# Kernel tuning notes

Hardware: AMD Instinct MI355X
Metric: run time of the kernel (lower is better)

The kernel has to match this reference:

```python
import jax, jax.numpy as jnp
import numpy as np

BITS = 4
GROUP = 128
PACK = 32 // BITS  # 8 values per int32
MASK = (1 << BITS) - 1


def _unpack_weight(qweight, K, N):
    # qweight: [K//PACK, N] int32; PACK 4-bit values packed along K in each int32
    shifts = jnp.arange(PACK, dtype=jnp.int32) * BITS  # [PACK]
    w = (qweight[:, None, :] >> shifts[None, :, None]) & MASK  # [K//PACK, PACK, N]
    return w.reshape(K, N)


def _unpack_zeros(qzeros, G, N):
    # qzeros: [G, N//PACK] int32; PACK 4-bit values packed along N in each int32
    shifts = jnp.arange(PACK, dtype=jnp.int32) * BITS  # [PACK]
    z = (qzeros[:, :, None] >> shifts[None, None, :]) & MASK  # [G, N//PACK, PACK]
    return z.reshape(G, N)


def setup_inputs() -> dict:
    key = jax.random.key(0)
    k1, k2, k3, k4 = jax.random.split(key, 4)
    B, S, K, N = 4, 1024, 4096, 11008
    G = K // GROUP
    x = jax.random.normal(k1, (B, S, K), dtype=jnp.float32)
    qweight = jax.random.randint(k2, (K // PACK, N), 0, 2147483647, dtype=jnp.int32)
    qzeros = jax.random.randint(k3, (G, N // PACK), 0, 2147483647, dtype=jnp.int32)
    scales = jax.random.uniform(k4, (G, N), dtype=jnp.float32) * 0.01
    return {"x": x, "qweight": qweight, "qzeros": qzeros, "scales": scales}


def reference(x, qweight, qzeros, scales):
    K = x.shape[-1]
    G, N = scales.shape
    # dequantize: W[k, n] = (q[k, n] - zero[g(k), n]) * scale[g(k), n]
    w_q = _unpack_weight(qweight, K, N).astype(jnp.float32)   # [K, N]
    zeros = _unpack_zeros(qzeros, G, N).astype(jnp.float32)   # [G, N]
    gid = jnp.arange(K) // GROUP                              # [K]
    W = (w_q - zeros[gid]) * scales[gid]                      # [K, N]
    return jnp.einsum('bsk,kn->bsn', x, W)
```

## Files before the change

### kernel.cpp

```cpp
#include <hip/hip_runtime.h>


#define BK 32
#define LDK 40
#define TILE_BYTES 10240

typedef _Float16 v8h __attribute__((ext_vector_type(8)));
typedef _Float16 half2v __attribute__((ext_vector_type(2)));
typedef float v4f __attribute__((ext_vector_type(4)));

__device__ __forceinline__ unsigned pkrtz_u32(float a, float b) {
  return __builtin_bit_cast(unsigned, __builtin_amdgcn_cvt_pkrtz(a, b));
}

__device__ __forceinline__ void load_lds_16B(const void* g, void* l) {
  __builtin_amdgcn_global_load_lds(
      (const __attribute__((address_space(1))) unsigned*)g,
      (__attribute__((address_space(3))) unsigned*)l, 16, 0, 0);
}

__device__ __forceinline__ void bar() { asm volatile("s_barrier" ::: "memory"); }

__global__ __launch_bounds__(512)
void prep_ab(const float* __restrict__ x,
             const unsigned* __restrict__ qweight,
             const unsigned* __restrict__ qzeros,
             const float* __restrict__ scales,
             unsigned short* __restrict__ fa,
             unsigned short* __restrict__ fb, int M, int N, int K) {
  const int KT = K / 64;
  const int NA = (M / 256) * KT;
  int b = blockIdx.x;
  if (b < NA) {
    const int mt = b / KT, t = b - mt * KT;
    unsigned short* tile = fa + (size_t)(mt * KT + t) * 16384;
#pragma unroll
    for (int p = 0; p < 4; ++p) {
      const int c = threadIdx.x + p * 512;
      const int h = c >> 10, r = (c >> 3) & 127, s = c & 7;
      const float* src = x + (size_t)(mt * 256 + h * 128 + r) * K + t * 64 + s * 8;
      const float4 v0 = ((const float4*)src)[0];
      const float4 v1 = ((const float4*)src)[1];
      uint4 o;
      o.x = pkrtz_u32(v0.x, v0.y); o.y = pkrtz_u32(v0.z, v0.w);
      o.z = pkrtz_u32(v1.x, v1.y); o.w = pkrtz_u32(v1.z, v1.w);
      *(uint4*)(tile + h * 8192 + r * 64 + ((s ^ (r & 7)) << 3)) = o;
    }
  } else {
    b -= NA;
    const int nt = b / KT, t = b - nt * KT;
    const int g = t >> 1;
    unsigned short* tile = fb + (size_t)(nt * KT + t) * 16384;
#pragma unroll
    for (int p = 0; p < 4; ++p) {
      const int c = threadIdx.x + p * 512;
      const int h = c >> 10, r = (c >> 3) & 127, s = c & 7;
      const int n = nt * 256 + h * 128 + r;
      const unsigned zp = qzeros[(size_t)g * (N >> 3) + (n >> 3)];
      const float sc = scales[(size_t)g * N + n];
      const unsigned z = (zp >> ((n & 7) * 4)) & 15u;
      const unsigned hz_u = 0x64006400u | z | (z << 16);
      const half2v hz2 = __builtin_bit_cast(half2v, hz_u);
      const half2v hs2 = __builtin_bit_cast(half2v, pkrtz_u32(sc, sc));
      const unsigned qv = qweight[(size_t)(t * 8 + s) * N + n];
      uint4 o;
      unsigned* wp = (unsigned*)&o;
#pragma unroll
      for (int bb = 0; bb < 4; ++bb) {
        const unsigned byte = qv >> (8 * bb);
        const unsigned pq = 0x64006400u | (byte & 0xFu) | ((byte & 0xF0u) << 12);
        const half2v w2 = (__builtin_bit_cast(half2v, pq) - hz2) * hs2;
        wp[bb] = __builtin_bit_cast(unsigned, w2);
      }
      *(uint4*)(tile + h * 8192 + r * 64 + ((s ^ (r & 7)) << 3)) = o;
    }
  }
}


#define READA4(PA, MB)                                                         \
  _Pragma("unroll") for (int i = 0; i < 4; ++i) {                              \
    aF[i][0] = *(const v8h*)((PA) + ((MB + i) * 16 + lr16) * 128 + koff0);     \
    aF[i][1] = *(const v8h*)((PA) + ((MB + i) * 16 + lr16) * 128 + koff1);     \
  }

#define READB2(PB, BF, NB)                                                     \
  _Pragma("unroll") for (int j = 0; j < 2; ++j) {                              \
    BF[j][0] = *(const v8h*)((PB) + ((NB + j) * 16 + lr16) * 128 + koff0);     \
    BF[j][1] = *(const v8h*)((PB) + ((NB + j) * 16 + lr16) * 128 + koff1);     \
  }

#define MMAQ(MB, NB, BF)                                                       \
  __builtin_amdgcn_s_setprio(1);                                              \
  _Pragma("unroll") for (int i = 0; i < 4; ++i)                                \
  _Pragma("unroll") for (int j = 0; j < 2; ++j) {                              \
    acc[MB + i][NB + j] = __builtin_amdgcn_mfma_f32_16x16x32_f16(              \
        aF[i][0], BF[j][0], acc[MB + i][NB + j], 0, 0, 0);                     \
    acc[MB + i][NB + j] = __builtin_amdgcn_mfma_f32_16x16x32_f16(              \
        aF[i][1], BF[j][1], acc[MB + i][NB + j], 0, 0, 0);                     \
  }                                                                            \
  __builtin_amdgcn_s_setprio(0);

__global__ __launch_bounds__(512, 2)
void qgemm8(const unsigned short* __restrict__ fa,
            const unsigned short* __restrict__ fb,
            float* __restrict__ out, int M, int N, int K) {
  __shared__ __align__(16) short As[2][2][128][64];
  __shared__ __align__(16) short Bs[2][2][128][64];

  const int tid = threadIdx.x;
  const int lane = tid & 63;
  const int wid = tid >> 6;
  const int wr = wid >> 2, wc = wid & 3;
  const int lr16 = lane & 15, hi4 = lane >> 4, l7 = lane & 7;
  const int koff0 = ((hi4 ^ l7) << 4);
  const int koff1 = (((4 + hi4) ^ l7) << 4);

  const int nmt = M / 256;
  const int nwg = nmt * (N / 256);
  int bid = blockIdx.x;
  {
    const int xcd = bid & 7, idx = bid >> 3;
    const int q = nwg >> 3, r = nwg & 7;
    bid = (xcd < r ? xcd * (q + 1) : r * (q + 1) + (xcd - r) * q) + idx;
  }
  const int mt = bid % nmt;
  const int nt = bid / nmt;

  const int NT = K / 64;
  const int NI = NT / 2;

  const char* srcA = (const char*)fa + (size_t)mt * NT * 32768 + wid * 1024 + lane * 16;
  const char* srcB = (const char*)fb + (size_t)nt * NT * 32768 + wid * 1024 + lane * 16;
  char* ldsA = (char*)&As[0][0][0][0];
  char* ldsB = (char*)&Bs[0][0][0][0];
  char* dstA = ldsA + wid * 1024;
  char* dstB = ldsB + wid * 1024;

  auto stageA = [&](int T, int h) {
    const char* s = srcA + (size_t)T * 32768 + h * 16384;
    char* d = dstA + (T & 1) * 32768 + h * 16384;
    load_lds_16B(s, d);
    load_lds_16B(s + 8192, d + 8192);
  };
  auto stageB = [&](int T, int h) {
    const char* s = srcB + (size_t)T * 32768 + h * 16384;
    char* d = dstB + (T & 1) * 32768 + h * 16384;
    load_lds_16B(s, d);
    load_lds_16B(s + 8192, d + 8192);
  };

  const char* pA[2] = {ldsA + wr * 16384, ldsA + 32768 + wr * 16384};
  const char* pB[2] = {ldsB + (wc >> 1) * 16384 + (wc & 1) * 8192,
                       ldsB + 32768 + (wc >> 1) * 16384 + (wc & 1) * 8192};

  v4f acc[8][4] = {};
  v8h aF[4][2], bL[2][2], bH[2][2];

  stageB(0, 0); stageB(0, 1); stageA(0, 0); stageA(0, 1);
  stageB(1, 0); stageB(1, 1);
  asm volatile("s_waitcnt vmcnt(4)");
  bar();

  for (int it = 0; it < NI; ++it) {
    const int t0 = 2 * it, t1 = 2 * it + 1;
    const bool pf = (it < NI - 1);

    READA4(pA[0], 0);
    READB2(pB[0], bL, 0);
    stageA(t1, 0);
    bar();
    MMAQ(0, 0, bL);
    READB2(pB[0], bH, 2);
    stageA(t1, 1);
    bar();
    MMAQ(0, 2, bH);
    READA4(pA[0], 4);
    bar();
    MMAQ(4, 0, bL);
    if (pf) { stageB(t0 + 2, 0); stageB(t0 + 2, 1);
              asm volatile("s_waitcnt vmcnt(4)"); }
    else    { asm volatile("s_waitcnt vmcnt(0)"); }
    bar();
    MMAQ(4, 2, bH);

    READA4(pA[1], 0);
    READB2(pB[1], bL, 0);
    if (pf) stageA(t0 + 2, 0);
    bar();
    MMAQ(0, 0, bL);
    READB2(pB[1], bH, 2);
    if (pf) stageA(t0 + 2, 1);
    bar();
    MMAQ(0, 2, bH);
    READA4(pA[1], 4);
    bar();
    MMAQ(4, 0, bL);
    if (pf) { stageB(t1 + 2, 0); stageB(t1 + 2, 1);
              asm volatile("s_waitcnt vmcnt(4)"); }
    else    { asm volatile("s_waitcnt vmcnt(0)"); }
    bar();
    MMAQ(4, 2, bH);
  }

  const int m0 = mt * 256 + wr * 128;
  const int n0 = nt * 256 + wc * 64;
#pragma unroll
  for (int mi = 0; mi < 8; ++mi) {
#pragma unroll
    for (int ni = 0; ni < 4; ++ni) {
#pragma unroll
      for (int r = 0; r < 4; ++r) {
        const int row = m0 + mi * 16 + hi4 * 4 + r;
        const int col = n0 + ni * 16 + lr16;
        out[(size_t)row * N + col] = acc[mi][ni][r];
      }
    }
  }
}

__global__ __launch_bounds__(320)
void prep_x(const float* __restrict__ x, unsigned short* __restrict__ xt, int K) {
  const int kt = blockIdx.x, mt = blockIdx.y;
  unsigned short* tile = xt + (size_t)(mt * (K / 32) + kt) * (TILE_BYTES / 2);
#pragma unroll
  for (int p = 0; p < 2; ++p) {
    const int c = threadIdx.x + p * 320;
    const int r = c / 5, j = c - r * 5;
    uint4 o = {0u, 0u, 0u, 0u};
    if (j < 4) {
      const float* src = x + (size_t)(mt * 128 + r) * K + kt * 32 + j * 8;
      const float4 v0 = ((const float4*)src)[0];
      const float4 v1 = ((const float4*)src)[1];
      o.x = pkrtz_u32(v0.x, v0.y); o.y = pkrtz_u32(v0.z, v0.w);
      o.z = pkrtz_u32(v1.x, v1.y); o.w = pkrtz_u32(v1.z, v1.w);
    }
    *(uint4*)((char*)tile + (size_t)c * 16) = o;
  }
}

__global__ __launch_bounds__(512, 4)
void qgemm_dma(const unsigned short* __restrict__ xt,
               const unsigned* __restrict__ qweight,
               const unsigned* __restrict__ qzeros,
               const float* __restrict__ scales,
               float* __restrict__ out, int M, int N, int K) {
  __shared__ __align__(16) short As[128][LDK];
  __shared__ __align__(16) short Bs[256][LDK];

  const int tid = threadIdx.x;
  const int lane = tid & 63;
  const int wid = tid >> 6;
  const int n0 = blockIdx.x * 256;
  const int m0 = blockIdx.y * 128;
  const int mt = blockIdx.y;
  const int wm = (wid >> 2) * 64;
  const int wn = (wid & 3) * 64;
  const int lr = lane & 15;
  const int lk = (lane >> 4) * 8;

  const int b_n = tid & 255;
  const int b_kr0 = tid >> 8;
  const int gn = n0 + b_n;
  const unsigned* qwb = qweight + (size_t)b_kr0 * N + gn;

  const char* xt_b = (const char*)xt;
  const int NT = K / BK;

  v4f acc[4][4] = {};

  unsigned b0c, b1c, zpc;
  float scc;
  auto load_b = [&](int t, unsigned& b0, unsigned& b1, unsigned& zp, float& sc) {
    const int kk = t * BK;
    const size_t qoff = (size_t)(kk >> 3) * N;
    b0 = qwb[qoff];
    b1 = qwb[qoff + 2 * (size_t)N];
    const int g = kk >> 7;
    zp = qzeros[(size_t)g * (N >> 3) + (gn >> 3)];
    sc = scales[(size_t)g * N + gn];
  };
  load_b(0, b0c, b1c, zpc, scc);

#pragma unroll 2
  for (int t = 0; t < NT; ++t) {
    {
      const char* g = xt_b + (size_t)(mt * NT + t) * TILE_BYTES +
                      (size_t)wid * 1024 + (size_t)lane * 16;
      char* l = ((char*)&As[0][0]) + wid * 1024;
      load_lds_16B(g, l);
      if (wid < 2) load_lds_16B(g + 8 * 1024, l + 8 * 1024);
    }
    {
      const unsigned z = (zpc >> ((gn & 7) * 4)) & 15u;
      const unsigned hz_u = 0x64006400u | z | (z << 16);
      const half2v hz2 = __builtin_bit_cast(half2v, hz_u);
      const half2v hs2 = __builtin_bit_cast(half2v, pkrtz_u32(scc, scc));
      const unsigned qvs[2] = {b0c, b1c};
#pragma unroll
      for (int q = 0; q < 2; ++q) {
        const int kr = b_kr0 + q * 2;
        const unsigned qv = qvs[q];
        uint4 wv;
        unsigned* wp = (unsigned*)&wv;
#pragma unroll
        for (int j = 0; j < 4; ++j) {
          const unsigned byte = qv >> (8 * j);
          const unsigned pq = 0x64006400u | (byte & 0xFu) | ((byte & 0xF0u) << 12);
          const half2v w2 = (__builtin_bit_cast(half2v, pq) - hz2) * hs2;
          wp[j] = __builtin_bit_cast(unsigned, w2);
        }
        *(uint4*)(&Bs[b_n][kr * 8]) = wv;
      }
    }

    __syncthreads();

    unsigned b0n, b1n, zpn;
    float scn;
    const int tn = (t + 1 < NT) ? (t + 1) : t;
    load_b(tn, b0n, b1n, zpn, scn);

    v8h af[4], bfr[4];
#pragma unroll
    for (int i = 0; i < 4; ++i) {
      af[i] = *(const v8h*)(&As[wm + i * 16 + lr][lk]);
      bfr[i] = *(const v8h*)(&Bs[wn + i * 16 + lr][lk]);
    }
#pragma unroll
    for (int mi = 0; mi < 4; ++mi) {
#pragma unroll
      for (int ni = 0; ni < 4; ++ni) {
        acc[mi][ni] = __builtin_amdgcn_mfma_f32_16x16x32_f16(
            af[mi], bfr[ni], acc[mi][ni], 0, 0, 0);
      }
    }

    __syncthreads();

    b0c = b0n; b1c = b1n; zpc = zpn; scc = scn;
  }

#pragma unroll
  for (int mi = 0; mi < 4; ++mi) {
#pragma unroll
    for (int ni = 0; ni < 4; ++ni) {
#pragma unroll
      for (int r = 0; r < 4; ++r) {
        const int row = m0 + wm + mi * 16 + (lane >> 4) * 4 + r;
        const int col = n0 + wn + ni * 16 + lr;
        out[(size_t)row * N + col] = acc[mi][ni][r];
      }
    }
  }
}

__global__ __launch_bounds__(256, 2)
void qgemm_fused(const float* __restrict__ x,
                 const unsigned* __restrict__ qweight,
                 const unsigned* __restrict__ qzeros,
                 const float* __restrict__ scales,
                 float* __restrict__ out, int M, int N, int K) {
  __shared__ short As[128][LDK];
  __shared__ short Bs[128][LDK];

  const int tid = threadIdx.x;
  const int lane = tid & 63;
  const int wid = tid >> 6;
  const int n0 = blockIdx.x * 128;
  const int m0 = blockIdx.y * 128;
  const int wm = (wid >> 1) * 64;
  const int wn = (wid & 1) * 64;
  const int lr = lane & 15;
  const int lk = (lane >> 4) * 8;

  const int a_row = tid >> 3;
  const int a_col = (tid & 7) * 4;
  const int b_n = tid & 127;
  const int b_kr0 = tid >> 7;
  const int gn = n0 + b_n;

  const float* xb = x + (size_t)(m0 + a_row) * K + a_col;
  const unsigned* qwb = qweight + (size_t)b_kr0 * N + gn;

  v4f acc[4][4] = {};
  const int NT = K / BK;

  float4 axc[4];
  unsigned b0c, b1c, zpc;
  float scc;

  auto load_step = [&](int t, float4 ax[4], unsigned& b0, unsigned& b1,
                       unsigned& zp, float& sc) {
    const int kk = t * BK;
#pragma unroll
    for (int p = 0; p < 4; ++p)
      ax[p] = *(const float4*)(xb + (size_t)(p * 32) * K + kk);
    const size_t qoff = (size_t)(kk >> 3) * N;
    b0 = qwb[qoff];
    b1 = qwb[qoff + 2 * (size_t)N];
    const int g = kk >> 7;
    zp = qzeros[(size_t)g * (N >> 3) + (gn >> 3)];
    sc = scales[(size_t)g * N + gn];
  };

  load_step(0, axc, b0c, b1c, zpc, scc);

#pragma unroll 2
  for (int t = 0; t < NT; ++t) {
    const unsigned z = (zpc >> ((gn & 7) * 4)) & 15u;
    const unsigned hz_u = 0x64006400u | z | (z << 16);
    const half2v hz2 = __builtin_bit_cast(half2v, hz_u);
    const half2v hs2 = __builtin_bit_cast(half2v, pkrtz_u32(scc, scc));

#pragma unroll
    for (int p = 0; p < 4; ++p) {
      const int row = p * 32 + a_row;
      uint2 pv;
      pv.x = pkrtz_u32(axc[p].x, axc[p].y);
      pv.y = pkrtz_u32(axc[p].z, axc[p].w);
      *(uint2*)(&As[row][a_col]) = pv;
    }
    {
      const unsigned qvs[2] = {b0c, b1c};
#pragma unroll
      for (int q = 0; q < 2; ++q) {
        const int kr = b_kr0 + q * 2;
        const unsigned qv = qvs[q];
        uint4 wv;
        unsigned* wp = (unsigned*)&wv;
#pragma unroll
        for (int j = 0; j < 4; ++j) {
          const unsigned byte = qv >> (8 * j);
          const unsigned pq = 0x64006400u | (byte & 0xFu) | ((byte & 0xF0u) << 12);
          const half2v w2 = (__builtin_bit_cast(half2v, pq) - hz2) * hs2;
          wp[j] = __builtin_bit_cast(unsigned, w2);
        }
        *(uint4*)(&Bs[b_n][kr * 8]) = wv;
      }
    }

    __syncthreads();

    float4 axn[4];
    unsigned b0n, b1n, zpn;
    float scn;
    const int tn = (t + 1 < NT) ? (t + 1) : t;
    load_step(tn, axn, b0n, b1n, zpn, scn);

    v8h af[4], bfr[4];
#pragma unroll
    for (int i = 0; i < 4; ++i) {
      af[i] = *(const v8h*)(&As[wm + i * 16 + lr][lk]);
      bfr[i] = *(const v8h*)(&Bs[wn + i * 16 + lr][lk]);
    }
#pragma unroll
    for (int mi = 0; mi < 4; ++mi) {
#pragma unroll
      for (int ni = 0; ni < 4; ++ni) {
        acc[mi][ni] = __builtin_amdgcn_mfma_f32_16x16x32_f16(
            af[mi], bfr[ni], acc[mi][ni], 0, 0, 0);
      }
    }

    __syncthreads();

#pragma unroll
    for (int p = 0; p < 4; ++p) axc[p] = axn[p];
    b0c = b0n; b1c = b1n; zpc = zpn; scc = scn;
  }

#pragma unroll
  for (int mi = 0; mi < 4; ++mi) {
#pragma unroll
    for (int ni = 0; ni < 4; ++ni) {
#pragma unroll
      for (int r = 0; r < 4; ++r) {
        const int row = m0 + wm + mi * 16 + (lane >> 4) * 4 + r;
        const int col = n0 + wn + ni * 16 + lr;
        out[(size_t)row * N + col] = acc[mi][ni][r];
      }
    }
  }
}

extern "C" void kernel_launch(void* const* d_in, const int* in_sizes, int n_in,
                              void* d_out, int out_size, void* d_ws, size_t ws_size,
                              hipStream_t stream) {
  const float* x = (const float*)d_in[0];
  const unsigned* qweight = (const unsigned*)d_in[1];
  const unsigned* qzeros = (const unsigned*)d_in[2];
  const float* scales = (const float*)d_in[3];
  float* out = (float*)d_out;

  const int K = 4096;
  const int N = 11008;
  const int M = in_sizes[0] / K;

  const size_t A8 = (size_t)(M / 256) * (K / 64) * 32768;
  const size_t B8 = (size_t)(N / 256) * (K / 64) * 32768;
  const size_t A_BYTES = (size_t)(M / 128) * (K / 32) * TILE_BYTES;

  if ((M % 256 == 0) && ws_size >= A8 + B8) {
    unsigned short* fa = (unsigned short*)d_ws;
    unsigned short* fb = (unsigned short*)((char*)d_ws + A8);
    const int nblk = (M / 256) * (K / 64) + (N / 256) * (K / 64);
    prep_ab<<<dim3(nblk), 512, 0, stream>>>(x, qweight, qzeros, scales, fa, fb, M, N, K);
    qgemm8<<<dim3((M / 256) * (N / 256)), 512, 0, stream>>>(fa, fb, out, M, N, K);
  } else if (ws_size >= A_BYTES) {
    unsigned short* xt = (unsigned short*)d_ws;
    prep_x<<<dim3(K / 32, M / 128), 320, 0, stream>>>(x, xt, K);
    qgemm_dma<<<dim3(N / 256, M / 128), 512, 0, stream>>>(xt, qweight, qzeros, scales,
                                                          out, M, N, K);
  } else {
    qgemm_fused<<<dim3(N / 128, M / 128), 256, 0, stream>>>(x, qweight, qzeros, scales,
                                                            out, M, N, K);
  }
}
```

Baseline: 587.3 us.

## Switch GEMM inner loop to 32x32x16 MFMA with precomputed LDS pointers

Replaces the 16x16x32 f16 MFMA tiling with 32x32x16 MFMA, so each wave computes its 128x64 tile as 4x2 blocks of 32x32 accumulators. LDS read addresses are precomputed once per buffer and k-slice, and global source pointers advance incrementally instead of being recomputed per stage. The larger MFMA shape needs fewer LDS fragment reads per FLOP and fewer instructions. In exchange the stage and barrier order changes, and the output store pattern moves to the 32x32 register layout.

```diff
diff --git a/kernel.cpp b/kernel.cpp
--- a/kernel.cpp
+++ b/kernel.cpp
@@ -8,6 +8,7 @@
 typedef _Float16 v8h __attribute__((ext_vector_type(8)));
 typedef _Float16 half2v __attribute__((ext_vector_type(2)));
 typedef float v4f __attribute__((ext_vector_type(4)));
+typedef float v16f __attribute__((ext_vector_type(16)));
 
 __device__ __forceinline__ unsigned pkrtz_u32(float a, float b) {
   return __builtin_bit_cast(unsigned, __builtin_amdgcn_cvt_pkrtz(a, b));
@@ -78,27 +79,23 @@
 }
 
 
-#define READA4(PA, MB)                                                         \
-  _Pragma("unroll") for (int i = 0; i < 4; ++i) {                              \
-    aF[i][0] = *(const v8h*)((PA) + ((MB + i) * 16 + lr16) * 128 + koff0);     \
-    aF[i][1] = *(const v8h*)((PA) + ((MB + i) * 16 + lr16) * 128 + koff1);     \
-  }
-
-#define READB2(PB, BF, NB)                                                     \
-  _Pragma("unroll") for (int j = 0; j < 2; ++j) {                              \
-    BF[j][0] = *(const v8h*)((PB) + ((NB + j) * 16 + lr16) * 128 + koff0);     \
-    BF[j][1] = *(const v8h*)((PB) + ((NB + j) * 16 + lr16) * 128 + koff1);     \
-  }
-
-#define MMAQ(MB, NB, BF)                                                       \
-  __builtin_amdgcn_s_setprio(1);                                              \
-  _Pragma("unroll") for (int i = 0; i < 4; ++i)                                \
-  _Pragma("unroll") for (int j = 0; j < 2; ++j) {                              \
-    acc[MB + i][NB + j] = __builtin_amdgcn_mfma_f32_16x16x32_f16(              \
-        aF[i][0], BF[j][0], acc[MB + i][NB + j], 0, 0, 0);                     \
-    acc[MB + i][NB + j] = __builtin_amdgcn_mfma_f32_16x16x32_f16(              \
-        aF[i][1], BF[j][1], acc[MB + i][NB + j], 0, 0, 0);                     \
-  }                                                                            \
+#define RDA(D, MB, KB2)                                                        \
+  _Pragma("unroll") for (int kk = 0; kk < 2; ++kk)                             \
+  _Pragma("unroll") for (int i = 0; i < 2; ++i)                                \
+    aF[i][kk] = *(const v8h*)(vA[D][(KB2) * 2 + kk] + ((MB) + i) * 4096);
+
+#define RDB(D, KB2, BF)                                                        \
+  _Pragma("unroll") for (int kk = 0; kk < 2; ++kk)                             \
+  _Pragma("unroll") for (int j = 0; j < 2; ++j)                                \
+    BF[j][kk] = *(const v8h*)(vB[D][(KB2) * 2 + kk] + j * 4096);
+
+#define MMA8(MB, BF)                                                           \
+  __builtin_amdgcn_s_setprio(1);                                               \
+  _Pragma("unroll") for (int kk = 0; kk < 2; ++kk)                             \
+  _Pragma("unroll") for (int i = 0; i < 2; ++i)                                \
+  _Pragma("unroll") for (int j = 0; j < 2; ++j)                                \
+    acc[(MB) + i][j] = __builtin_amdgcn_mfma_f32_32x32x16_f16(                 \
+        aF[i][kk], BF[j][kk], acc[(MB) + i][j], 0, 0, 0);                      \
   __builtin_amdgcn_s_setprio(0);
 
 __global__ __launch_bounds__(512, 2)
@@ -112,9 +109,7 @@
   const int lane = tid & 63;
   const int wid = tid >> 6;
   const int wr = wid >> 2, wc = wid & 3;
-  const int lr16 = lane & 15, hi4 = lane >> 4, l7 = lane & 7;
-  const int koff0 = ((hi4 ^ l7) << 4);
-  const int koff1 = (((4 + hi4) ^ l7) << 4);
+  const int r31 = lane & 31, l7 = lane & 7, hk = lane >> 5;
 
   const int nmt = M / 256;
   const int nwg = nmt * (N / 256);
@@ -130,93 +125,97 @@
   const int NT = K / 64;
   const int NI = NT / 2;
 
-  const char* srcA = (const char*)fa + (size_t)mt * NT * 32768 + wid * 1024 + lane * 16;
-  const char* srcB = (const char*)fb + (size_t)nt * NT * 32768 + wid * 1024 + lane * 16;
+  const char* sA = (const char*)fa + (size_t)mt * NT * 32768 + wid * 1024 + lane * 16;
+  const char* sB = (const char*)fb + (size_t)nt * NT * 32768 + wid * 1024 + lane * 16;
   char* ldsA = (char*)&As[0][0][0][0];
   char* ldsB = (char*)&Bs[0][0][0][0];
-  char* dstA = ldsA + wid * 1024;
-  char* dstB = ldsB + wid * 1024;
-
-  auto stageA = [&](int T, int h) {
-    const char* s = srcA + (size_t)T * 32768 + h * 16384;
-    char* d = dstA + (T & 1) * 32768 + h * 16384;
-    load_lds_16B(s, d);
-    load_lds_16B(s + 8192, d + 8192);
+  char* dA = ldsA + wid * 1024;
+  char* dB = ldsB + wid * 1024;
+
+  const char* vA[2][4];
+  const char* vB[2][4];
+#pragma unroll
+  for (int d = 0; d < 2; ++d)
+#pragma unroll
+    for (int kb = 0; kb < 4; ++kb) {
+      const int T = r31 * 128 + (((hk + 2 * kb) ^ l7) << 4);
+      vA[d][kb] = ldsA + d * 32768 + wr * 16384 + T;
+      vB[d][kb] = ldsB + d * 32768 + (wc >> 1) * 16384 + (wc & 1) * 8192 + T;
+    }
+
+  auto stA = [&](int so, int dof) {
+    load_lds_16B(sA + so, dA + dof);
+    load_lds_16B(sA + so + 8192, dA + dof + 8192);
   };
-  auto stageB = [&](int T, int h) {
-    const char* s = srcB + (size_t)T * 32768 + h * 16384;
-    char* d = dstB + (T & 1) * 32768 + h * 16384;
-    load_lds_16B(s, d);
-    load_lds_16B(s + 8192, d + 8192);
+  auto stB = [&](int so, int dof) {
+    load_lds_16B(sB + so, dB + dof);
+    load_lds_16B(sB + so + 8192, dB + dof + 8192);
   };
 
-  const char* pA[2] = {ldsA + wr * 16384, ldsA + 32768 + wr * 16384};
-  const char* pB[2] = {ldsB + (wc >> 1) * 16384 + (wc & 1) * 8192,
-                       ldsB + 32768 + (wc >> 1) * 16384 + (wc & 1) * 8192};
-
-  v4f acc[8][4] = {};
-  v8h aF[4][2], bL[2][2], bH[2][2];
-
-  stageB(0, 0); stageB(0, 1); stageA(0, 0); stageA(0, 1);
-  stageB(1, 0); stageB(1, 1);
+  v16f acc[4][2] = {};
+  v8h aF[2][2], bE[2][2], bO[2][2];
+
+  stB(0, 0); stB(16384, 16384);
+  stA(0, 0); stA(16384, 16384);
+  stB(32768, 32768); stB(49152, 49152);
   asm volatile("s_waitcnt vmcnt(4)");
   bar();
 
   for (int it = 0; it < NI; ++it) {
-    const int t0 = 2 * it, t1 = 2 * it + 1;
     const bool pf = (it < NI - 1);
 
-    READA4(pA[0], 0);
-    READB2(pB[0], bL, 0);
-    stageA(t1, 0);
-    bar();
-    MMAQ(0, 0, bL);
-    READB2(pB[0], bH, 2);
-    stageA(t1, 1);
-    bar();
-    MMAQ(0, 2, bH);
-    READA4(pA[0], 4);
-    bar();
-    MMAQ(4, 0, bL);
-    if (pf) { stageB(t0 + 2, 0); stageB(t0 + 2, 1);
+    RDA(0, 0, 0); RDB(0, 0, bE);
+    bar();
+    MMA8(0, bE);
+    RDA(0, 0, 1); RDB(0, 1, bO);
+    stA(32768, 32768);
+    bar();
+    MMA8(0, bO);
+    RDA(0, 2, 0);
+    stA(49152, 49152);
+    bar();
+    MMA8(2, bE);
+    RDA(0, 2, 1);
+    if (pf) { stB(65536, 0); stB(81920, 16384);
               asm volatile("s_waitcnt vmcnt(4)"); }
     else    { asm volatile("s_waitcnt vmcnt(0)"); }
     bar();
-    MMAQ(4, 2, bH);
-
-    READA4(pA[1], 0);
-    READB2(pB[1], bL, 0);
-    if (pf) stageA(t0 + 2, 0);
-    bar();
-    MMAQ(0, 0, bL);
-    READB2(pB[1], bH, 2);
-    if (pf) stageA(t0 + 2, 1);
-    bar();
-    MMAQ(0, 2, bH);
-    READA4(pA[1], 4);
-    bar();
-    MMAQ(4, 0, bL);
-    if (pf) { stageB(t1 + 2, 0); stageB(t1 + 2, 1);
+    MMA8(2, bO);
+
+    RDA(1, 0, 0); RDB(1, 0, bE);
+    bar();
+    MMA8(0, bE);
+    RDA(1, 0, 1); RDB(1, 1, bO);
+    if (pf) stA(65536, 0);
+    bar();
+    MMA8(0, bO);
+    RDA(1, 2, 0);
+    if (pf) stA(81920, 16384);
+    bar();
+    MMA8(2, bE);
+    RDA(1, 2, 1);
+    if (pf) { stB(98304, 32768); stB(114688, 49152);
               asm volatile("s_waitcnt vmcnt(4)"); }
     else    { asm volatile("s_waitcnt vmcnt(0)"); }
     bar();
-    MMAQ(4, 2, bH);
+    MMA8(2, bO);
+
+    sA += 65536; sB += 65536;
   }
 
   const int m0 = mt * 256 + wr * 128;
   const int n0 = nt * 256 + wc * 64;
-#pragma unroll
-  for (int mi = 0; mi < 8; ++mi) {
-#pragma unroll
-    for (int ni = 0; ni < 4; ++ni) {
-#pragma unroll
-      for (int r = 0; r < 4; ++r) {
-        const int row = m0 + mi * 16 + hi4 * 4 + r;
-        const int col = n0 + ni * 16 + lr16;
-        out[(size_t)row * N + col] = acc[mi][ni][r];
-      }
-    }
-  }
+  const int orow = 4 * hk;
+#pragma unroll
+  for (int mb = 0; mb < 4; ++mb)
+#pragma unroll
+    for (int nb = 0; nb < 2; ++nb)
+#pragma unroll
+      for (int reg = 0; reg < 16; ++reg) {
+        const int row = m0 + mb * 32 + orow + (reg & 3) + 8 * (reg >> 2);
+        const int col = n0 + nb * 32 + r31;
+        out[(size_t)row * N + col] = acc[mb][nb][reg];
+      }
 }
 
 __global__ __launch_bounds__(320)
```

New measurement: 597.5 us. About the same (+1.7%).
